# Optimization experiments

Hardware: AMD Instinct MI355X
Metric: run time of the kernel (lower is better)

The kernel has to match this reference:

```python
import jax, jax.numpy as jnp
import numpy as np

N_NODES = 200000
N_EDGES = 400000
N_GRAPHS = 4096
H = 300
L = 5
BN_EPS = 1e-5


def setup_inputs() -> dict:
    key = jax.random.key(0)
    ks = jax.random.split(key, 12)
    s = 0.05  # weight scale for numerical stability across 5 layers
    return {
        'x': jax.random.randint(ks[0], (N_NODES, 9), 0, 120),
        'edge_index': jax.random.randint(ks[1], (2, N_EDGES), 0, N_NODES),
        'edge_attr': jax.random.randint(ks[2], (N_EDGES, 3), 0, 16),
        'batch': jnp.sort(jax.random.randint(ks[3], (N_NODES,), 0, N_GRAPHS)),
        'atom_emb': jax.random.normal(ks[4], (9, 120, H), jnp.float32) * s,
        'bond_emb': jax.random.normal(ks[5], (L, 3, 16, H), jnp.float32) * s,
        'eps': jnp.zeros((L,), jnp.float32),
        'W1': jax.random.normal(ks[6], (L, H, 2 * H), jnp.float32) * s,
        'b1': jnp.zeros((L, 2 * H), jnp.float32),
        'bn_gamma': jnp.ones((L, 2 * H), jnp.float32),
        'bn_beta': jnp.zeros((L, 2 * H), jnp.float32),
        'bn_mean': jnp.zeros((L, 2 * H), jnp.float32),
        'bn_var': jnp.ones((L, 2 * H), jnp.float32),
        'W2': jax.random.normal(ks[7], (L, 2 * H, H), jnp.float32) * s,
        'b2': jnp.zeros((L, H), jnp.float32),
        'cls_W': jax.random.normal(ks[8], (H, 2), jnp.float32) * s,
        'cls_b': jnp.zeros((2,), jnp.float32),
    }


def reference(x, edge_index, edge_attr, batch, atom_emb, bond_emb, eps,
              W1, b1, bn_gamma, bn_beta, bn_mean, bn_var, W2, b2, cls_W, cls_b):
    N = x.shape[0]
    # AtomEncoder: sum of 9 categorical embeddings -> [N, H]
    h = jnp.sum(atom_emb[jnp.arange(9)[None, :], x], axis=1)
    src, dst = edge_index[0], edge_index[1]
    feat_idx3 = jnp.arange(3)[None, :]
    for l in range(W1.shape[0]):
        # BondEncoder for this layer: sum of 3 categorical embeddings -> [E, H]
        e = jnp.sum(bond_emb[l][feat_idx3, edge_attr], axis=1)
        # message = relu(x_j + edge_emb), aggregated by scatter-add at dst
        m = jax.nn.relu(h[src] + e)
        agg = jax.ops.segment_sum(m, dst, num_segments=N)
        z = (1.0 + eps[l]) * h + agg
        # MLP: Linear(H,2H) -> BN(eval) -> ReLU -> Linear(2H,H)
        z = z @ W1[l] + b1[l]
        z = (z - bn_mean[l]) * (bn_gamma[l] * jax.lax.rsqrt(bn_var[l] + BN_EPS)) + bn_beta[l]
        z = jax.nn.relu(z)
        h = z @ W2[l] + b2[l]
    # global mean pool over graphs
    sums = jax.ops.segment_sum(h, batch, num_segments=N_GRAPHS)
    counts = jax.ops.segment_sum(jnp.ones((N, 1), h.dtype), batch, num_segments=N_GRAPHS)
    graph_feature = sums / jnp.maximum(counts, 1.0)
    logits = graph_feature @ cls_W + cls_b
    return logits, graph_feature
```

## Files before the change

kernel.cpp:

```cpp
#include <hip/hip_runtime.h>
#include <hip/hip_bf16.h>

#define N_NODES 200000
#define N_EDGES 400000
#define N_GRAPHS 4096
#define HDIM 300
#define H2DIM 600
#define NLAYERS 5

typedef __hip_bfloat16 bf16;
typedef __attribute__((ext_vector_type(4))) short s16x4;
typedef __attribute__((ext_vector_type(8))) short s16x8;
typedef __attribute__((ext_vector_type(4))) float f32x4v;

__device__ inline short f2bf(float f) {
    __hip_bfloat16 b = __float2bfloat16(f);
    return *(short*)&b;
}
__device__ inline float bf2f(short s) {
    __hip_bfloat16 b = *(__hip_bfloat16*)&s;
    return __bfloat162float(b);
}

__global__ void diag_kernel(float* __restrict__ out, int n, float val) {
    int i = blockIdx.x * blockDim.x + threadIdx.x;
    if (i < n) out[i] = val;
}

__global__ void hist_kernel(const int* __restrict__ edge_index, int* __restrict__ offs) {
    int e = blockIdx.x * blockDim.x + threadIdx.x;
    if (e >= N_EDGES) return;
    atomicAdd(&offs[edge_index[N_EDGES + e]], 1);
}

#define SCAN_N 200001
__global__ void scan1_kernel(int* __restrict__ offs, int* __restrict__ bsum) {
    __shared__ int ls[256];
    int tid = threadIdx.x;
    int base = blockIdx.x * 1024 + tid * 4;
    int v[4];
#pragma unroll
    for (int j = 0; j < 4; j++) v[j] = (base + j < SCAN_N) ? offs[base + j] : 0;
    int t = v[0] + v[1] + v[2] + v[3];
    ls[tid] = t;
    __syncthreads();
    for (int off = 1; off < 256; off <<= 1) {
        int y = (tid >= off) ? ls[tid - off] : 0;
        __syncthreads();
        ls[tid] += y;
        __syncthreads();
    }
    int ex = ls[tid] - t;
#pragma unroll
    for (int j = 0; j < 4; j++) {
        if (base + j < SCAN_N) offs[base + j] = ex;
        ex += v[j];
    }
    if (tid == 255) bsum[blockIdx.x] = ls[255];
}

__global__ void scan2_kernel(int* __restrict__ bsum, int nb) {
    __shared__ int ls[256];
    int tid = threadIdx.x;
    int v = (tid < nb) ? bsum[tid] : 0;
    ls[tid] = v;
    __syncthreads();
    for (int off = 1; off < 256; off <<= 1) {
        int y = (tid >= off) ? ls[tid - off] : 0;
        __syncthreads();
        ls[tid] += y;
        __syncthreads();
    }
    if (tid < nb) bsum[tid] = ls[tid] - v;
}

__global__ void scan3_kernel(int* __restrict__ offs, const int* __restrict__ bsum) {
    int i = blockIdx.x * blockDim.x + threadIdx.x;
    if (i >= SCAN_N) return;
    offs[i] += bsum[i >> 10];
}

__global__ void scatter_kernel(const int* __restrict__ edge_index,
                               const int* __restrict__ edge_attr,
                               int* __restrict__ offs,
                               int* __restrict__ sidx) {
    int e = blockIdx.x * blockDim.x + threadIdx.x;
    if (e >= N_EDGES) return;
    int src = edge_index[e];
    int dst = edge_index[N_EDGES + e];
    int combo = edge_attr[e * 3 + 0] | (edge_attr[e * 3 + 1] << 4) | (edge_attr[e * 3 + 2] << 8);
    int pos = atomicAdd(&offs[dst], 1);
    sidx[pos] = src | (combo << 18);
}

__global__ void etab_kernel(const float* __restrict__ bond_l, short* __restrict__ etab) {
    int idx = blockIdx.x * blockDim.x + threadIdx.x;
    if (idx >= 4096 * 304) return;
    int combo = idx / 304;
    int c = idx - combo * 304;
    if (c >= HDIM) { etab[idx] = 0; return; }
    int a0 = combo & 15, a1 = (combo >> 4) & 15, a2 = combo >> 8;
    float v = bond_l[a0 * HDIM + c] + bond_l[16 * HDIM + a1 * HDIM + c]
            + bond_l[32 * HDIM + a2 * HDIM + c];
    etab[idx] = f2bf(v);
}

__global__ void prep_w_swz(const float* __restrict__ W1, const float* __restrict__ W2,
                           short* __restrict__ Wt1s, short* __restrict__ Wt2s) {
    int idx = blockIdx.x * blockDim.x + threadIdx.x;
    const int G1 = NLAYERS * 40 * 10 * 64;
    const int G2 = NLAYERS * 20 * 20 * 64;
    if (idx < G1) {
        int l = idx / (40 * 10 * 64);
        int r = idx - l * (40 * 10 * 64);
        int nt = r / (10 * 64);
        int r2 = r - nt * (10 * 64);
        int kb = r2 >> 6;
        int lane = r2 & 63;
        int n = nt * 16 + (lane & 15);
        int k0 = kb * 32 + (lane >> 4) * 8;
        s16x8 o;
#pragma unroll
        for (int j = 0; j < 8; j++) {
            int k = k0 + j;
            float v = (n < H2DIM && k < HDIM) ? W1[((size_t)l * HDIM + k) * H2DIM + n] : 0.f;
            o[j] = f2bf(v);
        }
        *(s16x8*)&Wt1s[(size_t)idx * 8] = o;
    } else if (idx < G1 + G2) {
        int t = idx - G1;
        int l = t / (20 * 20 * 64);
        int r = t - l * (20 * 20 * 64);
        int nt = r / (20 * 64);
        int r2 = r - nt * (20 * 64);
        int kb = r2 >> 6;
        int lane = r2 & 63;
        int n = nt * 16 + (lane & 15);
        int k0 = kb * 32 + (lane >> 4) * 8;
        s16x8 o;
#pragma unroll
        for (int j = 0; j < 8; j++) {
            int k = k0 + j;
            float v = (n < HDIM && k < H2DIM) ? W2[((size_t)l * H2DIM + k) * HDIM + n] : 0.f;
            o[j] = f2bf(v);
        }
        *(s16x8*)&Wt2s[(size_t)t * 8] = o;
    }
}

__global__ void atom_kernel(const int* __restrict__ x,
                            const float* __restrict__ atom_emb,
                            short* __restrict__ h) {
    int i = blockIdx.x * blockDim.x + threadIdx.x;
    if (i >= N_NODES * 75) return;
    int n = i / 75;
    int c = (i - n * 75) * 4;
    const int* xr = x + n * 9;
    float4 s = {0.f, 0.f, 0.f, 0.f};
#pragma unroll
    for (int f = 0; f < 9; f++) {
        float4 v = *(const float4*)&atom_emb[(size_t)(f * 120 + xr[f]) * HDIM + c];
        s.x += v.x; s.y += v.y; s.z += v.z; s.w += v.w;
    }
    s16x4 o = {f2bf(s.x), f2bf(s.y), f2bf(s.z), f2bf(s.w)};
    *(s16x4*)&h[(size_t)n * HDIM + c] = o;
}

__launch_bounds__(256)
__global__ void agg_kernel(const short* __restrict__ h_in,
                           short* __restrict__ z,
                           const int* __restrict__ offs,
                           const int* __restrict__ sidx,
                           const short* __restrict__ etab,
                           const float* __restrict__ eps, int l) {
    int tid = threadIdx.x;
    int q = tid >> 4;
    int l16 = tid & 15;
    int n = blockIdx.x * 16 + q;
    float e1 = 1.f + eps[l];
    int beg = (n == 0) ? 0 : offs[n - 1];
    int end = offs[n];

    float4 acc[5];
#pragma unroll
    for (int j = 0; j < 5; j++) acc[j] = (float4){0.f, 0.f, 0.f, 0.f};
    bool tail = l16 < 11;
    int ctail = 256 + l16 * 4;

    int e = beg;
    for (; e + 2 <= end; e += 2) {
        int pk0 = sidx[e];
        int pk1 = sidx[e + 1];
        const short* hr0 = h_in + (size_t)(pk0 & 0x3FFFF) * HDIM;
        const short* er0 = etab + (((unsigned)pk0) >> 18) * 304;
        const short* hr1 = h_in + (size_t)(pk1 & 0x3FFFF) * HDIM;
        const short* er1 = etab + (((unsigned)pk1) >> 18) * 304;
        s16x4 hv0[5], ev0[5], hv1[5], ev1[5];
#pragma unroll
        for (int rep = 0; rep < 4; rep++) {
            int c = rep * 64 + l16 * 4;
            hv0[rep] = *(const s16x4*)(hr0 + c);
            ev0[rep] = *(const s16x4*)(er0 + c);
            hv1[rep] = *(const s16x4*)(hr1 + c);
            ev1[rep] = *(const s16x4*)(er1 + c);
        }
        if (tail) {
            hv0[4] = *(const s16x4*)(hr0 + ctail);
            ev0[4] = *(const s16x4*)(er0 + ctail);
            hv1[4] = *(const s16x4*)(hr1 + ctail);
            ev1[4] = *(const s16x4*)(er1 + ctail);
        }
#pragma unroll
        for (int rep = 0; rep < 5; rep++) {
            if (rep == 4 && !tail) continue;
            acc[rep].x += fmaxf(0.f, bf2f(hv0[rep].x) + bf2f(ev0[rep].x))
                        + fmaxf(0.f, bf2f(hv1[rep].x) + bf2f(ev1[rep].x));
            acc[rep].y += fmaxf(0.f, bf2f(hv0[rep].y) + bf2f(ev0[rep].y))
                        + fmaxf(0.f, bf2f(hv1[rep].y) + bf2f(ev1[rep].y));
            acc[rep].z += fmaxf(0.f, bf2f(hv0[rep].z) + bf2f(ev0[rep].z))
                        + fmaxf(0.f, bf2f(hv1[rep].z) + bf2f(ev1[rep].z));
            acc[rep].w += fmaxf(0.f, bf2f(hv0[rep].w) + bf2f(ev0[rep].w))
                        + fmaxf(0.f, bf2f(hv1[rep].w) + bf2f(ev1[rep].w));
        }
    }
    if (e < end) {
        int pk0 = sidx[e];
        const short* hr0 = h_in + (size_t)(pk0 & 0x3FFFF) * HDIM;
        const short* er0 = etab + (((unsigned)pk0) >> 18) * 304;
        s16x4 hv0[5], ev0[5];
#pragma unroll
        for (int rep = 0; rep < 4; rep++) {
            int c = rep * 64 + l16 * 4;
            hv0[rep] = *(const s16x4*)(hr0 + c);
            ev0[rep] = *(const s16x4*)(er0 + c);
        }
        if (tail) {
            hv0[4] = *(const s16x4*)(hr0 + ctail);
            ev0[4] = *(const s16x4*)(er0 + ctail);
        }
#pragma unroll
        for (int rep = 0; rep < 5; rep++) {
            if (rep == 4 && !tail) continue;
            acc[rep].x += fmaxf(0.f, bf2f(hv0[rep].x) + bf2f(ev0[rep].x));
            acc[rep].y += fmaxf(0.f, bf2f(hv0[rep].y) + bf2f(ev0[rep].y));
            acc[rep].z += fmaxf(0.f, bf2f(hv0[rep].z) + bf2f(ev0[rep].z));
            acc[rep].w += fmaxf(0.f, bf2f(hv0[rep].w) + bf2f(ev0[rep].w));
        }
    }

    const short* hn = h_in + (size_t)n * HDIM;
    short* zr = z + (size_t)n * HDIM;
#pragma unroll
    for (int rep = 0; rep < 5; rep++) {
        if (rep == 4 && !tail) continue;
        int c = rep < 4 ? rep * 64 + l16 * 4 : ctail;
        s16x4 hv = *(const s16x4*)(hn + c);
        s16x4 o;
        o.x = f2bf(fmaf(e1, bf2f(hv.x), acc[rep].x));
        o.y = f2bf(fmaf(e1, bf2f(hv.y), acc[rep].y));
        o.z = f2bf(fmaf(e1, bf2f(hv.z), acc[rep].z));
        o.w = f2bf(fmaf(e1, bf2f(hv.w), acc[rep].w));
        *(s16x4*)(zr + c) = o;
    }
}

#define ZSTRIDE 320
#define YS_OFF (64 * ZSTRIDE)
#define YST 136
#define LDS_SHORTS (YS_OFF + 64 * YST)

__launch_bounds__(256, 2)
__global__ void mlp_kernel(const short* __restrict__ zin,
                           short* __restrict__ hout,
                           const short* __restrict__ Wt1,
                           const short* __restrict__ Wt2,
                           const float* __restrict__ b1l,
                           const float* __restrict__ gammal,
                           const float* __restrict__ betal,
                           const float* __restrict__ meanl,
                           const float* __restrict__ varl,
                           const float* __restrict__ b2l) {
    __shared__ short lds[LDS_SHORTS];
    int tid = threadIdx.x;
    int wng = tid >> 6;
    int lane = tid & 63;
    int quad = lane >> 4;
    int l16 = lane & 15;
    int row0 = blockIdx.x * 64;

    {
        const short* zbase = zin + (size_t)row0 * HDIM;
        for (int i = tid; i < 64 * 40; i += 256) {
            int r = i / 40;
            int cs = i - r * 40;
            const short* srcp = zbase + r * HDIM + cs * 8;
            s16x4 v0 = *(const s16x4*)srcp;
            s16x4 v1 = *(const s16x4*)(srcp + 4);
            int d = r * ZSTRIDE + ((cs ^ (r & 7)) << 3);
            *(s16x4*)&lds[d] = v0;
            *(s16x4*)&lds[d + 4] = v1;
        }
    }

    f32x4v acc2[4][5];
#pragma unroll
    for (int rt = 0; rt < 4; rt++)
#pragma unroll
        for (int ct = 0; ct < 5; ct++) acc2[rt][ct] = (f32x4v){0.f, 0.f, 0.f, 0.f};

    __syncthreads();

    for (int cc = 0; cc < 5; cc++) {
        f32x4v acc1[4][2];
#pragma unroll
        for (int rt = 0; rt < 4; rt++)
#pragma unroll
            for (int ct = 0; ct < 2; ct++) acc1[rt][ct] = (f32x4v){0.f, 0.f, 0.f, 0.f};

#pragma unroll
        for (int kb = 0; kb < 10; kb++) {
            s16x8 b[2];
#pragma unroll
            for (int ct = 0; ct < 2; ct++)
                b[ct] = *(const s16x8*)&Wt1[
                    ((size_t)(((cc * 8 + wng * 2 + ct) * 10 + kb) * 64) + lane) * 8];
            int ks = kb * 32 + quad * 8;
            s16x8 a[4];
#pragma unroll
            for (int rt = 0; rt < 4; rt++)
                a[rt] = *(const s16x8*)&lds[(rt * 16 + l16) * ZSTRIDE
                                            + (ks ^ ((l16 & 7) << 3))];
#pragma unroll
            for (int ct = 0; ct < 2; ct++)
#pragma unroll
                for (int rt = 0; rt < 4; rt++)
                    acc1[rt][ct] = __builtin_amdgcn_mfma_f32_16x16x32_bf16(
                        a[rt], b[ct], acc1[rt][ct], 0, 0, 0);
        }
        __syncthreads();
#pragma unroll
        for (int ct = 0; ct < 2; ct++) {
            int kc = wng * 32 + ct * 16 + l16;
            int col = cc * 128 + kc;
            bool valid = col < H2DIM;
            float s = 0.f, sh = 0.f;
            if (valid) {
                s = gammal[col] * rsqrtf(varl[col] + 1e-5f);
                sh = betal[col] + (b1l[col] - meanl[col]) * s;
            }
#pragma unroll
            for (int rt = 0; rt < 4; rt++)
#pragma unroll
                for (int rr = 0; rr < 4; rr++) {
                    float v = valid ? fmaxf(0.f, fmaf(acc1[rt][ct][rr], s, sh)) : 0.f;
                    lds[YS_OFF + (rt * 16 + quad * 4 + rr) * YST + kc] = f2bf(v);
                }
        }
        __syncthreads();
#pragma unroll
        for (int kbl = 0; kbl < 4; kbl++) {
            s16x8 b[5];
#pragma unroll
            for (int ct = 0; ct < 5; ct++)
                b[ct] = *(const s16x8*)&Wt2[
                    ((size_t)(((wng * 5 + ct) * 20 + cc * 4 + kbl) * 64) + lane) * 8];
            int ks = kbl * 32 + quad * 8;
            s16x8 a[4];
#pragma unroll
            for (int rt = 0; rt < 4; rt++)
                a[rt] = *(const s16x8*)&lds[YS_OFF + (rt * 16 + l16) * YST + ks];
#pragma unroll
            for (int ct = 0; ct < 5; ct++)
#pragma unroll
                for (int rt = 0; rt < 4; rt++)
                    acc2[rt][ct] = __builtin_amdgcn_mfma_f32_16x16x32_bf16(
                        a[rt], b[ct], acc2[rt][ct], 0, 0, 0);
        }
    }

#pragma unroll
    for (int ct = 0; ct < 5; ct++) {
        int col = wng * 80 + ct * 16 + l16;
        if (col < HDIM) {
            float bb = b2l[col];
#pragma unroll
            for (int rt = 0; rt < 4; rt++)
#pragma unroll
                for (int rr = 0; rr < 4; rr++) {
                    int rrow = rt * 16 + quad * 4 + rr;
                    lds[rrow * HDIM + col] = f2bf(acc2[rt][ct][rr] + bb);
                }
        }
    }
    __syncthreads();
    for (int i = tid; i < 64 * 75; i += 256) {
        *(s16x4*)&hout[(size_t)row0 * HDIM + i * 4] = *(const s16x4*)&lds[i * 4];
    }
}

__device__ int lower_bound_dev(const int* a, int n, int v) {
    int lo = 0, hi = n;
    while (lo < hi) {
        int mid = (lo + hi) >> 1;
        if (a[mid] < v) lo = mid + 1; else hi = mid;
    }
    return lo;
}

__global__ void pool_kernel(const short* __restrict__ h,
                            const int* __restrict__ batch,
                            const float* __restrict__ cls_W,
                            const float* __restrict__ cls_b,
                            float* __restrict__ out) {
    __shared__ int seg[2];
    __shared__ float r0s[256], r1s[256];
    int g = blockIdx.x;
    int t = threadIdx.x;
    if (t == 0) {
        seg[0] = lower_bound_dev(batch, N_NODES, g);
        seg[1] = lower_bound_dev(batch, N_NODES, g + 1);
    }
    __syncthreads();
    int s = seg[0], e = seg[1];
    float inv = 1.f / fmaxf((float)(e - s), 1.f);
    float p0 = 0.f, p1 = 0.f;
    if (t < 75) {
        int c = t * 4;
        float4 sum = {0.f, 0.f, 0.f, 0.f};
        for (int n = s; n < e; n++) {
            s16x4 v = *(const s16x4*)&h[(size_t)n * HDIM + c];
            sum.x += bf2f(v.x);
            sum.y += bf2f(v.y);
            sum.z += bf2f(v.z);
            sum.w += bf2f(v.w);
        }
        float4 gf = {sum.x * inv, sum.y * inv, sum.z * inv, sum.w * inv};
        *(float4*)&out[2 * N_GRAPHS + (size_t)g * HDIM + c] = gf;
        p0 = gf.x * cls_W[c * 2] + gf.y * cls_W[(c + 1) * 2]
           + gf.z * cls_W[(c + 2) * 2] + gf.w * cls_W[(c + 3) * 2];
        p1 = gf.x * cls_W[c * 2 + 1] + gf.y * cls_W[(c + 1) * 2 + 1]
           + gf.z * cls_W[(c + 2) * 2 + 1] + gf.w * cls_W[(c + 3) * 2 + 1];
    }
    r0s[t] = p0;
    r1s[t] = p1;
    __syncthreads();
    for (int st = 128; st > 0; st >>= 1) {
        if (t < st) { r0s[t] += r0s[t + st]; r1s[t] += r1s[t + st]; }
        __syncthreads();
    }
    if (t == 0) {
        out[g * 2 + 0] = r0s[0] + cls_b[0];
        out[g * 2 + 1] = r1s[0] + cls_b[1];
    }
}

extern "C" void kernel_launch(void* const* d_in, const int* in_sizes, int n_in,
                              void* d_out, int out_size, void* d_ws, size_t ws_size,
                              hipStream_t stream) {
    const int* x          = (const int*)d_in[0];
    const int* edge_index = (const int*)d_in[1];
    const int* edge_attr  = (const int*)d_in[2];
    const int* batch      = (const int*)d_in[3];
    const float* atom_emb = (const float*)d_in[4];
    const float* bond_emb = (const float*)d_in[5];
    const float* eps      = (const float*)d_in[6];
    const float* W1       = (const float*)d_in[7];
    const float* b1       = (const float*)d_in[8];
    const float* bn_gamma = (const float*)d_in[9];
    const float* bn_beta  = (const float*)d_in[10];
    const float* bn_mean  = (const float*)d_in[11];
    const float* bn_var   = (const float*)d_in[12];
    const float* W2       = (const float*)d_in[13];
    const float* b2       = (const float*)d_in[14];
    const float* cls_W    = (const float*)d_in[15];
    const float* cls_b    = (const float*)d_in[16];
    float* out = (float*)d_out;

    char* base = (char*)d_ws;
    const size_t OFF_HA   = 0;
    const size_t OFF_HB   = 120000000;
    const size_t OFF_WT1  = 240000000;
    const size_t OFF_WT2  = 242048000;
    const size_t OFF_ETAB = 244096000;
    const size_t OFF_SIDX = 246586368;
    const size_t OFF_OFFS = 248186368;
    const size_t OFF_BSUM = 248986384;
    const size_t TOTAL    = 248987168;

    if (ws_size < TOTAL) {
        float mb = (float)(ws_size >> 20);
        diag_kernel<<<(out_size + 255) / 256, 256, 0, stream>>>(out, out_size, mb);
        return;
    }

    short* hA   = (short*)(base + OFF_HA);
    short* hB   = (short*)(base + OFF_HB);
    short* Wt1s = (short*)(base + OFF_WT1);
    short* Wt2s = (short*)(base + OFF_WT2);
    short* etab = (short*)(base + OFF_ETAB);
    int*   sidx = (int*)(base + OFF_SIDX);
    int*   offs = (int*)(base + OFF_OFFS);
    int*   bsum = (int*)(base + OFF_BSUM);

    hipMemsetAsync(offs, 0, SCAN_N * sizeof(int), stream);
    hist_kernel<<<(N_EDGES + 255) / 256, 256, 0, stream>>>(edge_index, offs);
    scan1_kernel<<<196, 256, 0, stream>>>(offs, bsum);
    scan2_kernel<<<1, 256, 0, stream>>>(bsum, 196);
    scan3_kernel<<<(SCAN_N + 255) / 256, 256, 0, stream>>>(offs, bsum);
    scatter_kernel<<<(N_EDGES + 255) / 256, 256, 0, stream>>>(edge_index, edge_attr, offs, sidx);

    {
        int total = NLAYERS * 40 * 10 * 64 + NLAYERS * 20 * 20 * 64;
        prep_w_swz<<<(total + 255) / 256, 256, 0, stream>>>(W1, W2, Wt1s, Wt2s);
    }
    atom_kernel<<<(N_NODES * 75 + 255) / 256, 256, 0, stream>>>(x, atom_emb, hA);

    for (int l = 0; l < NLAYERS; l++) {
        etab_kernel<<<(4096 * 304 + 255) / 256, 256, 0, stream>>>(
            bond_emb + (size_t)l * 3 * 16 * HDIM, etab);
        agg_kernel<<<N_NODES / 16, 256, 0, stream>>>(
            hA, hB, offs, sidx, etab, eps, l);
        mlp_kernel<<<N_NODES / 64, 256, 0, stream>>>(
            hB, hA,
            Wt1s + (size_t)l * 640 * 320, Wt2s + (size_t)l * 320 * 640,
            b1 + l * H2DIM, bn_gamma + l * H2DIM, bn_beta + l * H2DIM,
            bn_mean + l * H2DIM, bn_var + l * H2DIM, b2 + l * HDIM);
    }

    pool_kernel<<<N_GRAPHS, 256, 0, stream>>>(hA, batch, cls_W, cls_b, out);
}
```

Before: 2.267 ms.

## Read MLP input A-tiles from global memory and shrink LDS for higher occupancy

The MLP kernel no longer stages the 64x300 input tile in LDS and instead loads the A fragments for the first GEMM directly from global memory, relying on cache. The output staging is split into two 32-row halves, which shrinks shared memory so launch bounds can go from 2 to 3 blocks per SM. The aim is more resident waves and fewer barriers. The cost is unswizzled global loads repeated per column chunk, which read the input five times through cache, plus extra syncs in the epilogue. The 3-block bound may also cause register spills.

```diff
diff --git a/kernel.cpp b/kernel.cpp
--- a/kernel.cpp
+++ b/kernel.cpp
@@ -264,12 +264,12 @@
     }
 }
 
-#define ZSTRIDE 320
-#define YS_OFF (64 * ZSTRIDE)
 #define YST 136
-#define LDS_SHORTS (YS_OFF + 64 * YST)
-
-__launch_bounds__(256, 2)
+#define YS_SHORTS (64 * YST)
+#define HST_OFF YS_SHORTS
+#define LDS_SHORTS (YS_SHORTS + 32 * HDIM)
+
+__launch_bounds__(256, 3)
 __global__ void mlp_kernel(const short* __restrict__ zin,
                            short* __restrict__ hout,
                            const short* __restrict__ Wt1,
@@ -287,28 +287,13 @@
     int quad = lane >> 4;
     int l16 = lane & 15;
     int row0 = blockIdx.x * 64;
-
-    {
-        const short* zbase = zin + (size_t)row0 * HDIM;
-        for (int i = tid; i < 64 * 40; i += 256) {
-            int r = i / 40;
-            int cs = i - r * 40;
-            const short* srcp = zbase + r * HDIM + cs * 8;
-            s16x4 v0 = *(const s16x4*)srcp;
-            s16x4 v1 = *(const s16x4*)(srcp + 4);
-            int d = r * ZSTRIDE + ((cs ^ (r & 7)) << 3);
-            *(s16x4*)&lds[d] = v0;
-            *(s16x4*)&lds[d + 4] = v1;
-        }
-    }
+    const short* zrow = zin + (size_t)row0 * HDIM;
 
     f32x4v acc2[4][5];
 #pragma unroll
     for (int rt = 0; rt < 4; rt++)
 #pragma unroll
         for (int ct = 0; ct < 5; ct++) acc2[rt][ct] = (f32x4v){0.f, 0.f, 0.f, 0.f};
-
-    __syncthreads();
 
     for (int cc = 0; cc < 5; cc++) {
         f32x4v acc1[4][2];
@@ -328,8 +313,7 @@
             s16x8 a[4];
 #pragma unroll
             for (int rt = 0; rt < 4; rt++)
-                a[rt] = *(const s16x8*)&lds[(rt * 16 + l16) * ZSTRIDE
-                                            + (ks ^ ((l16 & 7) << 3))];
+                a[rt] = *(const s16x8*)&zrow[(size_t)(rt * 16 + l16) * HDIM + ks];
 #pragma unroll
             for (int ct = 0; ct < 2; ct++)
 #pragma unroll
@@ -353,7 +337,7 @@
 #pragma unroll
                 for (int rr = 0; rr < 4; rr++) {
                     float v = valid ? fmaxf(0.f, fmaf(acc1[rt][ct][rr], s, sh)) : 0.f;
-                    lds[YS_OFF + (rt * 16 + quad * 4 + rr) * YST + kc] = f2bf(v);
+                    lds[(rt * 16 + quad * 4 + rr) * YST + kc] = f2bf(v);
                 }
         }
         __syncthreads();
@@ -368,7 +352,7 @@
             s16x8 a[4];
 #pragma unroll
             for (int rt = 0; rt < 4; rt++)
-                a[rt] = *(const s16x8*)&lds[YS_OFF + (rt * 16 + l16) * YST + ks];
+                a[rt] = *(const s16x8*)&lds[(rt * 16 + l16) * YST + ks];
 #pragma unroll
             for (int ct = 0; ct < 5; ct++)
 #pragma unroll
@@ -379,22 +363,29 @@
     }
 
 #pragma unroll
-    for (int ct = 0; ct < 5; ct++) {
-        int col = wng * 80 + ct * 16 + l16;
-        if (col < HDIM) {
-            float bb = b2l[col];
-#pragma unroll
-            for (int rt = 0; rt < 4; rt++)
-#pragma unroll
-                for (int rr = 0; rr < 4; rr++) {
-                    int rrow = rt * 16 + quad * 4 + rr;
-                    lds[rrow * HDIM + col] = f2bf(acc2[rt][ct][rr] + bb);
+    for (int half = 0; half < 2; half++) {
+#pragma unroll
+        for (int rt2 = 0; rt2 < 2; rt2++) {
+            int rt = half * 2 + rt2;
+#pragma unroll
+            for (int ct = 0; ct < 5; ct++) {
+                int col = wng * 80 + ct * 16 + l16;
+                if (col < HDIM) {
+                    float bb = b2l[col];
+#pragma unroll
+                    for (int rr = 0; rr < 4; rr++) {
+                        int rrow = rt2 * 16 + quad * 4 + rr;
+                        lds[HST_OFF + rrow * HDIM + col] = f2bf(acc2[rt][ct][rr] + bb);
+                    }
                 }
-        }
-    }
-    __syncthreads();
-    for (int i = tid; i < 64 * 75; i += 256) {
-        *(s16x4*)&hout[(size_t)row0 * HDIM + i * 4] = *(const s16x4*)&lds[i * 4];
+            }
+        }
+        __syncthreads();
+        for (int i = tid; i < 32 * 75; i += 256) {
+            *(s16x4*)&hout[(size_t)(row0 + half * 32) * HDIM + i * 4] =
+                *(const s16x4*)&lds[HST_OFF + i * 4];
+        }
+        if (half == 0) __syncthreads();
     }
 }
 
```

Result: slower. 5.196 ms (+129.2%).

## Fuse edge aggregation into MLP kernel, writing aggregated rows directly to LDS

Applied to the files above, without the earlier changes.

The separate aggregation kernel is removed and its gather-relu-sum loop is moved into the MLP kernel. Each block now aggregates its 64 rows into the swizzled LDS tile before the GEMMs, so the intermediate z tensor is never written to or read back from global memory, and one launch per layer goes away. Because input and output can no longer alias, h ping-pongs between two buffers, and the pool reads the final buffer. The cost is that the latency-bound gather now runs inside a kernel limited to two blocks per CU, which may hide memory latency less well than the standalone kernel did.

```diff
diff --git a/kernel.cpp b/kernel.cpp
--- a/kernel.cpp
+++ b/kernel.cpp
@@ -166,112 +166,18 @@
     *(s16x4*)&h[(size_t)n * HDIM + c] = o;
 }
 
-__launch_bounds__(256)
-__global__ void agg_kernel(const short* __restrict__ h_in,
-                           short* __restrict__ z,
-                           const int* __restrict__ offs,
-                           const int* __restrict__ sidx,
-                           const short* __restrict__ etab,
-                           const float* __restrict__ eps, int l) {
-    int tid = threadIdx.x;
-    int q = tid >> 4;
-    int l16 = tid & 15;
-    int n = blockIdx.x * 16 + q;
-    float e1 = 1.f + eps[l];
-    int beg = (n == 0) ? 0 : offs[n - 1];
-    int end = offs[n];
-
-    float4 acc[5];
-#pragma unroll
-    for (int j = 0; j < 5; j++) acc[j] = (float4){0.f, 0.f, 0.f, 0.f};
-    bool tail = l16 < 11;
-    int ctail = 256 + l16 * 4;
-
-    int e = beg;
-    for (; e + 2 <= end; e += 2) {
-        int pk0 = sidx[e];
-        int pk1 = sidx[e + 1];
-        const short* hr0 = h_in + (size_t)(pk0 & 0x3FFFF) * HDIM;
-        const short* er0 = etab + (((unsigned)pk0) >> 18) * 304;
-        const short* hr1 = h_in + (size_t)(pk1 & 0x3FFFF) * HDIM;
-        const short* er1 = etab + (((unsigned)pk1) >> 18) * 304;
-        s16x4 hv0[5], ev0[5], hv1[5], ev1[5];
-#pragma unroll
-        for (int rep = 0; rep < 4; rep++) {
-            int c = rep * 64 + l16 * 4;
-            hv0[rep] = *(const s16x4*)(hr0 + c);
-            ev0[rep] = *(const s16x4*)(er0 + c);
-            hv1[rep] = *(const s16x4*)(hr1 + c);
-            ev1[rep] = *(const s16x4*)(er1 + c);
-        }
-        if (tail) {
-            hv0[4] = *(const s16x4*)(hr0 + ctail);
-            ev0[4] = *(const s16x4*)(er0 + ctail);
-            hv1[4] = *(const s16x4*)(hr1 + ctail);
-            ev1[4] = *(const s16x4*)(er1 + ctail);
-        }
-#pragma unroll
-        for (int rep = 0; rep < 5; rep++) {
-            if (rep == 4 && !tail) continue;
-            acc[rep].x += fmaxf(0.f, bf2f(hv0[rep].x) + bf2f(ev0[rep].x))
-                        + fmaxf(0.f, bf2f(hv1[rep].x) + bf2f(ev1[rep].x));
-            acc[rep].y += fmaxf(0.f, bf2f(hv0[rep].y) + bf2f(ev0[rep].y))
-                        + fmaxf(0.f, bf2f(hv1[rep].y) + bf2f(ev1[rep].y));
-            acc[rep].z += fmaxf(0.f, bf2f(hv0[rep].z) + bf2f(ev0[rep].z))
-                        + fmaxf(0.f, bf2f(hv1[rep].z) + bf2f(ev1[rep].z));
-            acc[rep].w += fmaxf(0.f, bf2f(hv0[rep].w) + bf2f(ev0[rep].w))
-                        + fmaxf(0.f, bf2f(hv1[rep].w) + bf2f(ev1[rep].w));
-        }
-    }
-    if (e < end) {
-        int pk0 = sidx[e];
-        const short* hr0 = h_in + (size_t)(pk0 & 0x3FFFF) * HDIM;
-        const short* er0 = etab + (((unsigned)pk0) >> 18) * 304;
-        s16x4 hv0[5], ev0[5];
-#pragma unroll
-        for (int rep = 0; rep < 4; rep++) {
-            int c = rep * 64 + l16 * 4;
-            hv0[rep] = *(const s16x4*)(hr0 + c);
-            ev0[rep] = *(const s16x4*)(er0 + c);
-        }
-        if (tail) {
-            hv0[4] = *(const s16x4*)(hr0 + ctail);
-            ev0[4] = *(const s16x4*)(er0 + ctail);
-        }
-#pragma unroll
-        for (int rep = 0; rep < 5; rep++) {
-            if (rep == 4 && !tail) continue;
-            acc[rep].x += fmaxf(0.f, bf2f(hv0[rep].x) + bf2f(ev0[rep].x));
-            acc[rep].y += fmaxf(0.f, bf2f(hv0[rep].y) + bf2f(ev0[rep].y));
-            acc[rep].z += fmaxf(0.f, bf2f(hv0[rep].z) + bf2f(ev0[rep].z));
-            acc[rep].w += fmaxf(0.f, bf2f(hv0[rep].w) + bf2f(ev0[rep].w));
-        }
-    }
-
-    const short* hn = h_in + (size_t)n * HDIM;
-    short* zr = z + (size_t)n * HDIM;
-#pragma unroll
-    for (int rep = 0; rep < 5; rep++) {
-        if (rep == 4 && !tail) continue;
-        int c = rep < 4 ? rep * 64 + l16 * 4 : ctail;
-        s16x4 hv = *(const s16x4*)(hn + c);
-        s16x4 o;
-        o.x = f2bf(fmaf(e1, bf2f(hv.x), acc[rep].x));
-        o.y = f2bf(fmaf(e1, bf2f(hv.y), acc[rep].y));
-        o.z = f2bf(fmaf(e1, bf2f(hv.z), acc[rep].z));
-        o.w = f2bf(fmaf(e1, bf2f(hv.w), acc[rep].w));
-        *(s16x4*)(zr + c) = o;
-    }
-}
-
 #define ZSTRIDE 320
 #define YS_OFF (64 * ZSTRIDE)
 #define YST 136
 #define LDS_SHORTS (YS_OFF + 64 * YST)
 
 __launch_bounds__(256, 2)
-__global__ void mlp_kernel(const short* __restrict__ zin,
-                           short* __restrict__ hout,
+__global__ void mlp_kernel(const short* __restrict__ hIn,
+                           short* __restrict__ hOut,
+                           const int* __restrict__ offs,
+                           const int* __restrict__ sidx,
+                           const short* __restrict__ etab,
+                           const float* __restrict__ eps, int l,
                            const short* __restrict__ Wt1,
                            const short* __restrict__ Wt2,
                            const float* __restrict__ b1l,
@@ -285,20 +191,105 @@
     int wng = tid >> 6;
     int lane = tid & 63;
     int quad = lane >> 4;
-    int l16 = lane & 15;
+    int l16 = tid & 15;
+    int q = tid >> 4;
     int row0 = blockIdx.x * 64;
-
-    {
-        const short* zbase = zin + (size_t)row0 * HDIM;
-        for (int i = tid; i < 64 * 40; i += 256) {
-            int r = i / 40;
-            int cs = i - r * 40;
-            const short* srcp = zbase + r * HDIM + cs * 8;
-            s16x4 v0 = *(const s16x4*)srcp;
-            s16x4 v1 = *(const s16x4*)(srcp + 4);
-            int d = r * ZSTRIDE + ((cs ^ (r & 7)) << 3);
-            *(s16x4*)&lds[d] = v0;
-            *(s16x4*)&lds[d + 4] = v1;
+    float e1 = 1.f + eps[l];
+
+    bool tail = l16 < 11;
+    int ctail = 256 + l16 * 4;
+#pragma unroll 1
+    for (int g = 0; g < 4; g++) {
+        int r = g * 16 + q;
+        int n = row0 + r;
+        int beg = (n == 0) ? 0 : offs[n - 1];
+        int end = offs[n];
+
+        float4 acc[5];
+#pragma unroll
+        for (int j = 0; j < 5; j++) acc[j] = (float4){0.f, 0.f, 0.f, 0.f};
+
+        int e = beg;
+        for (; e + 2 <= end; e += 2) {
+            int pk0 = sidx[e];
+            int pk1 = sidx[e + 1];
+            const short* hr0 = hIn + (size_t)(pk0 & 0x3FFFF) * HDIM;
+            const short* er0 = etab + (((unsigned)pk0) >> 18) * 304;
+            const short* hr1 = hIn + (size_t)(pk1 & 0x3FFFF) * HDIM;
+            const short* er1 = etab + (((unsigned)pk1) >> 18) * 304;
+            s16x4 hv0[5], ev0[5], hv1[5], ev1[5];
+#pragma unroll
+            for (int rep = 0; rep < 4; rep++) {
+                int c = rep * 64 + l16 * 4;
+                hv0[rep] = *(const s16x4*)(hr0 + c);
+                ev0[rep] = *(const s16x4*)(er0 + c);
+                hv1[rep] = *(const s16x4*)(hr1 + c);
+                ev1[rep] = *(const s16x4*)(er1 + c);
+            }
+            if (tail) {
+                hv0[4] = *(const s16x4*)(hr0 + ctail);
+                ev0[4] = *(const s16x4*)(er0 + ctail);
+                hv1[4] = *(const s16x4*)(hr1 + ctail);
+                ev1[4] = *(const s16x4*)(er1 + ctail);
+            }
+#pragma unroll
+            for (int rep = 0; rep < 5; rep++) {
+                if (rep == 4 && !tail) continue;
+                acc[rep].x += fmaxf(0.f, bf2f(hv0[rep].x) + bf2f(ev0[rep].x))
+                            + fmaxf(0.f, bf2f(hv1[rep].x) + bf2f(ev1[rep].x));
+                acc[rep].y += fmaxf(0.f, bf2f(hv0[rep].y) + bf2f(ev0[rep].y))
+                            + fmaxf(0.f, bf2f(hv1[rep].y) + bf2f(ev1[rep].y));
+                acc[rep].z += fmaxf(0.f, bf2f(hv0[rep].z) + bf2f(ev0[rep].z))
+                            + fmaxf(0.f, bf2f(hv1[rep].z) + bf2f(ev1[rep].z));
+                acc[rep].w += fmaxf(0.f, bf2f(hv0[rep].w) + bf2f(ev0[rep].w))
+                            + fmaxf(0.f, bf2f(hv1[rep].w) + bf2f(ev1[rep].w));
+            }
+        }
+        if (e < end) {
+            int pk0 = sidx[e];
+            const short* hr0 = hIn + (size_t)(pk0 & 0x3FFFF) * HDIM;
+            const short* er0 = etab + (((unsigned)pk0) >> 18) * 304;
+            s16x4 hv0[5], ev0[5];
+#pragma unroll
+            for (int rep = 0; rep < 4; rep++) {
+                int c = rep * 64 + l16 * 4;
+                hv0[rep] = *(const s16x4*)(hr0 + c);
+                ev0[rep] = *(const s16x4*)(er0 + c);
+            }
+            if (tail) {
+                hv0[4] = *(const s16x4*)(hr0 + ctail);
+                ev0[4] = *(const s16x4*)(er0 + ctail);
+            }
+#pragma unroll
+            for (int rep = 0; rep < 5; rep++) {
+                if (rep == 4 && !tail) continue;
+                acc[rep].x += fmaxf(0.f, bf2f(hv0[rep].x) + bf2f(ev0[rep].x));
+                acc[rep].y += fmaxf(0.f, bf2f(hv0[rep].y) + bf2f(ev0[rep].y));
+                acc[rep].z += fmaxf(0.f, bf2f(hv0[rep].z) + bf2f(ev0[rep].z));
+                acc[rep].w += fmaxf(0.f, bf2f(hv0[rep].w) + bf2f(ev0[rep].w));
+            }
+        }
+
+        const short* hn = hIn + (size_t)n * HDIM;
+#pragma unroll
+        for (int rep = 0; rep < 5; rep++) {
+            if (rep == 4 && !tail) continue;
+            int c = rep < 4 ? rep * 64 + l16 * 4 : ctail;
+            s16x4 hv = *(const s16x4*)(hn + c);
+            s16x4 o;
+            o.x = f2bf(fmaf(e1, bf2f(hv.x), acc[rep].x));
+            o.y = f2bf(fmaf(e1, bf2f(hv.y), acc[rep].y));
+            o.z = f2bf(fmaf(e1, bf2f(hv.z), acc[rep].z));
+            o.w = f2bf(fmaf(e1, bf2f(hv.w), acc[rep].w));
+            int cs = c >> 3;
+            int d = r * ZSTRIDE + (((cs ^ (r & 7)) << 3) | (c & 7));
+            *(s16x4*)&lds[d] = o;
+        }
+        if (l16 >= 11) {
+            int c = 300 + (l16 - 11) * 4;
+            int cs = c >> 3;
+            int d = r * ZSTRIDE + (((cs ^ (r & 7)) << 3) | (c & 7));
+            *(s16x4*)&lds[d] = (s16x4){0, 0, 0, 0};
         }
     }
 
@@ -394,7 +385,7 @@
     }
     __syncthreads();
     for (int i = tid; i < 64 * 75; i += 256) {
-        *(s16x4*)&hout[(size_t)row0 * HDIM + i * 4] = *(const s16x4*)&lds[i * 4];
+        *(s16x4*)&hOut[(size_t)row0 * HDIM + i * 4] = *(const s16x4*)&lds[i * 4];
     }
 }
 
@@ -518,14 +509,14 @@
     for (int l = 0; l < NLAYERS; l++) {
         etab_kernel<<<(4096 * 304 + 255) / 256, 256, 0, stream>>>(
             bond_emb + (size_t)l * 3 * 16 * HDIM, etab);
-        agg_kernel<<<N_NODES / 16, 256, 0, stream>>>(
-            hA, hB, offs, sidx, etab, eps, l);
+        const short* hin = (l & 1) ? hB : hA;
+        short* hout = (l & 1) ? hA : hB;
         mlp_kernel<<<N_NODES / 64, 256, 0, stream>>>(
-            hB, hA,
+            hin, hout, offs, sidx, etab, eps, l,
             Wt1s + (size_t)l * 640 * 320, Wt2s + (size_t)l * 320 * 640,
             b1 + l * H2DIM, bn_gamma + l * H2DIM, bn_beta + l * H2DIM,
             bn_mean + l * H2DIM, bn_var + l * H2DIM, b2 + l * HDIM);
     }
 
-    pool_kernel<<<N_GRAPHS, 256, 0, stream>>>(hA, batch, cls_W, cls_b, out);
-}
+    pool_kernel<<<N_GRAPHS, 256, 0, stream>>>(hB, batch, cls_W, cls_b, out);
+}
```

Result: slower. 2.322 ms (+2.4%).
